# Kernel optimization log

Hardware: AMD Instinct MI355X
Metric: run time of the kernel (lower is better)

## Reference

```python
import jax, jax.numpy as jnp
import numpy as np

B, C_IN, C_OUT, H, W = 16, 256, 256, 64, 64
RANK, ORDER = 16, 2
EPS = 1e-5


def setup_inputs() -> dict:
    key = jax.random.key(0)
    k1, k2, k3 = jax.random.split(key, 3)
    x = jax.random.normal(k1, (B, C_IN, H, W), dtype=jnp.float32)
    # torch init: w_core ~ N(0, 1/(C_in*rank)), w_out ~ N(0, 1/rank)
    w_core = jax.random.normal(k2, (RANK, C_IN, RANK), dtype=jnp.float32) * (1.0 / (C_IN * RANK))
    w_out = jax.random.normal(k3, (RANK, C_OUT, RANK), dtype=jnp.float32) * (1.0 / RANK)
    return {"x": x, "w_core": w_core, "w_out": w_out}


def reference(x, w_core, w_out):
    # Per-pixel tensor-ring 1x1 conv.
    # Original chain for order=2 (share_core):
    #   T = einsum('achw,rck->arhwk', x, w_core)
    #   out = einsum('aebcf,afbcg,gdh->aedbch', T, T, w_out)
    #   y   = einsum('arohwr->aohw', out)   # ring trace over e==h
    # Equivalent: M[a,h,w] is rank x rank; P = M^order; y_d = tr(P @ W_d)
    M = jnp.einsum('achw,rck->ahwrk', x, w_core)  # [B,H,W,r,r]
    P = M
    for _ in range(ORDER - 1):
        P = jnp.einsum('ahwef,ahwfg->ahweg', P, M)
    y = jnp.einsum('ahweg,gde->adhw', P, w_out)  # [B,C_out,H,W]
    # InstanceNorm2d (affine=False, biased variance) + Softsign
    mean = jnp.mean(y, axis=(2, 3), keepdims=True)
    var = jnp.var(y, axis=(2, 3), keepdims=True)
    yn = (y - mean) * jax.lax.rsqrt(var + EPS)
    return yn / (1.0 + jnp.abs(yn))
```

## Files before the change

kernel.cpp:

```cpp
#include <hip/hip_runtime.h>

#define HW 4096
#define NC 256
#define ND 256
#define NB 16

typedef _Float16 half2_t __attribute__((ext_vector_type(2)));
typedef _Float16 half4_t __attribute__((ext_vector_type(4)));
typedef _Float16 half8_t __attribute__((ext_vector_type(8)));
typedef __fp16   fp16x2  __attribute__((ext_vector_type(2)));
typedef float floatx2 __attribute__((ext_vector_type(2)));
typedef float floatx4 __attribute__((ext_vector_type(4)));

#define MSCALE 64.0f
#define INV_MSCALE2 (1.0f / 4096.0f)
#define EPS_SCALED (1e-5f * 4096.0f * 4096.0f)

__global__ __launch_bounds__(256) void prep_weights(
        const float* __restrict__ w_core, const float* __restrict__ w_out,
        _Float16* __restrict__ W1p, _Float16* __restrict__ W2p,
        float* __restrict__ ssum) {
    int tid = blockIdx.x * 256 + threadIdx.x;
    if (tid < 8192) ssum[tid] = 0.f;
    int l   = tid & 63;
    int rt  = (tid >> 6) & 15;
    int ks  = (tid >> 10) & 7;
    int sel = tid >> 13;
    int row = l & 15, kg = l >> 4;
    half8_t v;
    if (sel == 0) {
        int r = rt, k = row;
#pragma unroll
        for (int j = 0; j < 8; ++j) {
            int c = ks * 32 + kg * 8 + j;
            v[j] = (_Float16)(w_core[r * 4096 + c * 16 + k] * MSCALE);
        }
        *(half8_t*)&W1p[(size_t)((ks * 16 + rt) * 64 + l) * 8] = v;
    } else {
        int d = rt * 16 + row;
#pragma unroll
        for (int j = 0; j < 8; ++j) {
            int eg = ks * 32 + kg * 8 + j, e = eg >> 4, g = eg & 15;
            v[j] = (_Float16)w_out[g * 4096 + d * 16 + e];
        }
        *(half8_t*)&W2p[(size_t)((ks * 16 + rt) * 64 + l) * 8] = v;
    }
}

template<bool F16Y>
__global__ __launch_bounds__(256, 2) void compute_y(
        const float* __restrict__ x, const _Float16* __restrict__ W1p,
        const _Float16* __restrict__ W2p, float* __restrict__ y,
        _Float16* __restrict__ y16, float* __restrict__ ssum,
        float* __restrict__ ssq) {
    __shared__ __align__(16) float S[16384];
    _Float16* XT  = (_Float16*)S;
    float*    Mf  = S;
    _Float16* PLb = (_Float16*)S;

    const int t = threadIdx.x;
    const int l = t & 63, w = t >> 6;
    const int a = blockIdx.x >> 6;
    const int pixbase = (blockIdx.x & 63) * 64;
    const int row16 = l & 15, kg = l >> 4;
    const float* xa = x + (size_t)a * NC * HW + pixbase;

    {
        const int px = t & 63;
        const int o0 = t >> 6;
#pragma unroll
        for (int q = 0; q < 8; ++q) {
            const int oct = q * 4 + o0;
            half8_t hv;
#pragma unroll
            for (int j = 0; j < 8; ++j)
                hv[j] = (_Float16)xa[(size_t)(oct * 8 + j) * HW + px];
            *(half8_t*)&XT[px * 256 + ((oct ^ (px & 15)) << 3)] = hv;
        }
    }
    __syncthreads();

    floatx4 acc[4][4];
#pragma unroll
    for (int i = 0; i < 4; ++i)
#pragma unroll
        for (int j = 0; j < 4; ++j) acc[i][j] = (floatx4){0.f, 0.f, 0.f, 0.f};
    {
        const half8_t* W1v = (const half8_t*)W1p;
        half8_t af[4], afn[4];
#pragma unroll
        for (int rq = 0; rq < 4; ++rq) af[rq] = W1v[(w * 4 + rq) * 64 + l];
        for (int ks = 0; ks < 8; ++ks) {
            if (ks < 7) {
#pragma unroll
                for (int rq = 0; rq < 4; ++rq)
                    afn[rq] = W1v[((ks + 1) * 16 + w * 4 + rq) * 64 + l];
            }
#pragma unroll
            for (int pt = 0; pt < 4; ++pt) {
                const int px = pt * 16 + row16;
                half8_t bf = *(const half8_t*)
                    &XT[px * 256 + (((ks * 4 + kg) ^ row16) << 3)];
#pragma unroll
                for (int rq = 0; rq < 4; ++rq)
                    acc[rq][pt] = __builtin_amdgcn_mfma_f32_16x16x32_f16(
                                      af[rq], bf, acc[rq][pt], 0, 0, 0);
            }
#pragma unroll
            for (int rq = 0; rq < 4; ++rq) af[rq] = afn[rq];
        }
    }

    const half8_t* W2v = (const half8_t*)W2p;
    half8_t caf[4], cafn[4];
#pragma unroll
    for (int dq = 0; dq < 4; ++dq) caf[dq] = W2v[(w * 4 + dq) * 64 + l];

    __syncthreads();

#pragma unroll
    for (int rq = 0; rq < 4; ++rq) {
        const int u = (w * 4 + rq) * 4 + kg;
#pragma unroll
        for (int pt = 0; pt < 4; ++pt) {
            const int px = pt * 16 + row16;
            *(floatx4*)&Mf[px * 256 + ((u ^ row16) << 2)] = acc[rq][pt];
        }
    }
    __syncthreads();

    {
        const int p = t >> 2, qe = t & 3, ps = p & 15;
        const float* Mp = &Mf[p * 256];
        float Af[4][16];
#pragma unroll
        for (int i = 0; i < 4; ++i) {
            const int e = i * 4 + qe;
#pragma unroll
            for (int f4 = 0; f4 < 4; ++f4) {
                floatx4 v = *(const floatx4*)&Mp[(((e * 4 + f4) ^ ps) << 2)];
#pragma unroll
                for (int j = 0; j < 4; ++j) Af[i][f4 * 4 + j] = v[j];
            }
        }
        floatx2 Pacc[4][8];
#pragma unroll
        for (int i = 0; i < 4; ++i)
#pragma unroll
            for (int g2 = 0; g2 < 8; ++g2) Pacc[i][g2] = (floatx2){0.f, 0.f};
#pragma unroll
        for (int f = 0; f < 16; ++f) {
            floatx2 Bg[8];
#pragma unroll
            for (int g4 = 0; g4 < 4; ++g4) {
                floatx4 v = *(const floatx4*)&Mp[(((f * 4 + g4) ^ ps) << 2)];
                Bg[g4 * 2]     = (floatx2){v[0], v[1]};
                Bg[g4 * 2 + 1] = (floatx2){v[2], v[3]};
            }
#pragma unroll
            for (int i = 0; i < 4; ++i) {
                floatx2 a2 = {Af[i][f], Af[i][f]};
#pragma unroll
                for (int g2 = 0; g2 < 8; ++g2)
                    Pacc[i][g2] = __builtin_elementwise_fma(a2, Bg[g2], Pacc[i][g2]);
            }
        }
#pragma unroll
        for (int i = 0; i < 4; ++i) {
            const int e = i * 4 + qe;
#pragma unroll
            for (int h2 = 0; h2 < 2; ++h2) {
                half8_t hv;
#pragma unroll
                for (int g2 = 0; g2 < 4; ++g2) {
                    fp16x2 pk = __builtin_amdgcn_cvt_pkrtz(
                        Pacc[i][h2 * 4 + g2][0], Pacc[i][h2 * 4 + g2][1]);
                    hv[g2 * 2]     = (_Float16)pk[0];
                    hv[g2 * 2 + 1] = (_Float16)pk[1];
                }
                *(half8_t*)&PLb[p * 512 + (((e * 2 + h2) ^ ps) << 3)] = hv;
            }
        }
    }
    __syncthreads();

    floatx4 cacc[4][4];
#pragma unroll
    for (int i = 0; i < 4; ++i)
#pragma unroll
        for (int j = 0; j < 4; ++j) cacc[i][j] = (floatx4){0.f, 0.f, 0.f, 0.f};
    for (int ks = 0; ks < 8; ++ks) {
        if (ks < 7) {
#pragma unroll
            for (int dq = 0; dq < 4; ++dq)
                cafn[dq] = W2v[((ks + 1) * 16 + w * 4 + dq) * 64 + l];
        }
#pragma unroll
        for (int pt = 0; pt < 4; ++pt) {
            const int px = pt * 16 + row16;
            half8_t bf = *(const half8_t*)
                &PLb[px * 512 + (((ks * 4 + kg) ^ row16) << 3)];
#pragma unroll
            for (int dq = 0; dq < 4; ++dq)
                cacc[dq][pt] = __builtin_amdgcn_mfma_f32_16x16x32_f16(
                                   caf[dq], bf, cacc[dq][pt], 0, 0, 0);
        }
#pragma unroll
        for (int dq = 0; dq < 4; ++dq) caf[dq] = cafn[dq];
    }

    float*     ya   = y   + (size_t)a * ND * HW + pixbase;
    _Float16*  ya16 = F16Y ? (y16 + (size_t)a * ND * HW + pixbase) : nullptr;
#pragma unroll
    for (int dq = 0; dq < 4; ++dq) {
        const int dbase = (w * 4 + dq) * 16 + kg * 4;
#pragma unroll
        for (int r2 = 0; r2 < 4; ++r2) {
            const int d = dbase + r2;
            float s = 0.f, q2 = 0.f;
#pragma unroll
            for (int pt = 0; pt < 4; ++pt) {
                float v;
                if (F16Y) {
                    _Float16 hv = (_Float16)cacc[dq][pt][r2];
                    ya16[(size_t)d * HW + pt * 16 + row16] = hv;
                    v = (float)hv;
                } else {
                    v = cacc[dq][pt][r2] * INV_MSCALE2;
                    ya[(size_t)d * HW + pt * 16 + row16] = v;
                }
                s += v; q2 += v * v;
            }
#pragma unroll
            for (int off = 1; off < 16; off <<= 1) {
                s  += __shfl_xor(s, off);
                q2 += __shfl_xor(q2, off);
            }
            if (row16 == 0) {
                atomicAdd(&ssum[a * 256 + d], s);
                atomicAdd(&ssq [a * 256 + d], q2);
            }
        }
    }
}

__global__ __launch_bounds__(256) void finalize_f16(
        const _Float16* __restrict__ y16, const float* __restrict__ ssum,
        const float* __restrict__ ssq, float* __restrict__ out) {
    const int ad = blockIdx.x;
    const float m  = ssum[ad] * (1.f / HW);
    const float sv = ssq[ad] * (1.f / HW) - m * m;
    const float s  = rsqrtf(sv + EPS_SCALED);
    const size_t base = (size_t)ad * HW + threadIdx.x * 16;
    half8_t h0 = *(const half8_t*)&y16[base];
    half8_t h1 = *(const half8_t*)&y16[base + 8];
    float o[16];
#pragma unroll
    for (int j = 0; j < 8; ++j) {
        float z0 = ((float)h0[j] - m) * s;
        float z1 = ((float)h1[j] - m) * s;
        o[j]     = z0 / (1.f + fabsf(z0));
        o[8 + j] = z1 / (1.f + fabsf(z1));
    }
#pragma unroll
    for (int q = 0; q < 4; ++q)
        *(float4*)&out[base + q * 4] =
            make_float4(o[q * 4], o[q * 4 + 1], o[q * 4 + 2], o[q * 4 + 3]);
}

__global__ __launch_bounds__(256) void finalize_f32(
        float* __restrict__ y, const float* __restrict__ ssum,
        const float* __restrict__ ssq) {
    const int i4 = blockIdx.x * 256 + threadIdx.x;
    const int ad = i4 >> 10;
    const float m  = ssum[ad] * (1.f / HW);
    const float sv = ssq[ad] * (1.f / HW) - m * m;
    const float s  = rsqrtf(sv + 1e-5f);
    float4 v = ((const float4*)y)[i4];
    float vv[4] = {v.x, v.y, v.z, v.w};
#pragma unroll
    for (int lq = 0; lq < 4; ++lq) {
        float z = (vv[lq] - m) * s;
        vv[lq] = z / (1.f + fabsf(z));
    }
    ((float4*)y)[i4] = make_float4(vv[0], vv[1], vv[2], vv[3]);
}

extern "C" void kernel_launch(void* const* d_in, const int* in_sizes, int n_in,
                              void* d_out, int out_size, void* d_ws, size_t ws_size,
                              hipStream_t stream) {
    const float* x      = (const float*)d_in[0];
    const float* w_core = (const float*)d_in[1];
    const float* w_out  = (const float*)d_in[2];
    float* y = (float*)d_out;

    char* wsb = (char*)d_ws;
    _Float16* W1p = (_Float16*)wsb;
    _Float16* W2p = (_Float16*)(wsb + 131072);
    float* ssum   = (float*)(wsb + 262144);
    float* ssq    = (float*)(wsb + 278528);
    _Float16* y16 = (_Float16*)(wsb + 294912);

    const size_t need_f16 = 294912 + (size_t)NB * ND * HW * sizeof(_Float16);
    const bool use_f16 = ws_size >= need_f16;

    prep_weights<<<64, 256, 0, stream>>>(w_core, w_out, W1p, W2p, ssum);
    if (use_f16) {
        compute_y<true><<<1024, 256, 0, stream>>>(x, W1p, W2p, y, y16, ssum, ssq);
        finalize_f16<<<4096, 256, 0, stream>>>(y16, ssum, ssq, y);
    } else {
        compute_y<false><<<1024, 256, 0, stream>>>(x, W1p, W2p, y, nullptr, ssum, ssq);
        finalize_f32<<<16384, 256, 0, stream>>>(y, ssum, ssq);
    }
}
```

Before: 82.50 us.

## Store intermediate M in fp16 LDS to halve shared memory and batch x loads

The shared buffer shrinks from 64KB of float to 32KB of half, so M is stored as fp16 and converted back to float for the per-pixel 16x16 matrix square. This lowers LDS use per block and may allow more resident blocks. The x staging now issues 32 global loads before converting, which gives more memory-level parallelism, and the W1 fragment prefetch is hoisted ahead of the x load. Keeping M in fp16 loses some precision, and the restructured loops raise register pressure.

```diff
diff --git a/kernel.cpp b/kernel.cpp
--- a/kernel.cpp
+++ b/kernel.cpp
@@ -53,10 +53,7 @@
         const _Float16* __restrict__ W2p, float* __restrict__ y,
         _Float16* __restrict__ y16, float* __restrict__ ssum,
         float* __restrict__ ssq) {
-    __shared__ __align__(16) float S[16384];
-    _Float16* XT  = (_Float16*)S;
-    float*    Mf  = S;
-    _Float16* PLb = (_Float16*)S;
+    __shared__ __align__(16) _Float16 S[16384];
 
     const int t = threadIdx.x;
     const int l = t & 63, w = t >> 6;
@@ -65,17 +62,32 @@
     const int row16 = l & 15, kg = l >> 4;
     const float* xa = x + (size_t)a * NC * HW + pixbase;
 
+    const half8_t* W1v = (const half8_t*)W1p;
+    half8_t af[4], afn[4];
+#pragma unroll
+    for (int rq = 0; rq < 4; ++rq) af[rq] = W1v[(w * 4 + rq) * 64 + l];
+
     {
         const int px = t & 63;
         const int o0 = t >> 6;
 #pragma unroll
-        for (int q = 0; q < 8; ++q) {
-            const int oct = q * 4 + o0;
-            half8_t hv;
-#pragma unroll
-            for (int j = 0; j < 8; ++j)
-                hv[j] = (_Float16)xa[(size_t)(oct * 8 + j) * HW + px];
-            *(half8_t*)&XT[px * 256 + ((oct ^ (px & 15)) << 3)] = hv;
+        for (int h = 0; h < 2; ++h) {
+            float xr[32];
+#pragma unroll
+            for (int q = 0; q < 4; ++q) {
+                const int oct = (h * 4 + q) * 4 + o0;
+#pragma unroll
+                for (int j = 0; j < 8; ++j)
+                    xr[q * 8 + j] = xa[(size_t)(oct * 8 + j) * HW + px];
+            }
+#pragma unroll
+            for (int q = 0; q < 4; ++q) {
+                const int oct = (h * 4 + q) * 4 + o0;
+                half8_t hv;
+#pragma unroll
+                for (int j = 0; j < 8; ++j) hv[j] = (_Float16)xr[q * 8 + j];
+                *(half8_t*)&S[px * 256 + ((oct ^ (px & 15)) << 3)] = hv;
+            }
         }
     }
     __syncthreads();
@@ -85,30 +97,24 @@
     for (int i = 0; i < 4; ++i)
 #pragma unroll
         for (int j = 0; j < 4; ++j) acc[i][j] = (floatx4){0.f, 0.f, 0.f, 0.f};
-    {
-        const half8_t* W1v = (const half8_t*)W1p;
-        half8_t af[4], afn[4];
-#pragma unroll
-        for (int rq = 0; rq < 4; ++rq) af[rq] = W1v[(w * 4 + rq) * 64 + l];
-        for (int ks = 0; ks < 8; ++ks) {
-            if (ks < 7) {
-#pragma unroll
-                for (int rq = 0; rq < 4; ++rq)
-                    afn[rq] = W1v[((ks + 1) * 16 + w * 4 + rq) * 64 + l];
-            }
-#pragma unroll
-            for (int pt = 0; pt < 4; ++pt) {
-                const int px = pt * 16 + row16;
-                half8_t bf = *(const half8_t*)
-                    &XT[px * 256 + (((ks * 4 + kg) ^ row16) << 3)];
-#pragma unroll
-                for (int rq = 0; rq < 4; ++rq)
-                    acc[rq][pt] = __builtin_amdgcn_mfma_f32_16x16x32_f16(
-                                      af[rq], bf, acc[rq][pt], 0, 0, 0);
-            }
-#pragma unroll
-            for (int rq = 0; rq < 4; ++rq) af[rq] = afn[rq];
-        }
+    for (int ks = 0; ks < 8; ++ks) {
+        if (ks < 7) {
+#pragma unroll
+            for (int rq = 0; rq < 4; ++rq)
+                afn[rq] = W1v[((ks + 1) * 16 + w * 4 + rq) * 64 + l];
+        }
+#pragma unroll
+        for (int pt = 0; pt < 4; ++pt) {
+            const int px = pt * 16 + row16;
+            half8_t bf = *(const half8_t*)
+                &S[px * 256 + (((ks * 4 + kg) ^ row16) << 3)];
+#pragma unroll
+            for (int rq = 0; rq < 4; ++rq)
+                acc[rq][pt] = __builtin_amdgcn_mfma_f32_16x16x32_f16(
+                                  af[rq], bf, acc[rq][pt], 0, 0, 0);
+        }
+#pragma unroll
+        for (int rq = 0; rq < 4; ++rq) af[rq] = afn[rq];
     }
 
     const half8_t* W2v = (const half8_t*)W2p;
@@ -124,45 +130,52 @@
 #pragma unroll
         for (int pt = 0; pt < 4; ++pt) {
             const int px = pt * 16 + row16;
-            *(floatx4*)&Mf[px * 256 + ((u ^ row16) << 2)] = acc[rq][pt];
+            half4_t hv;
+#pragma unroll
+            for (int r2 = 0; r2 < 4; ++r2) hv[r2] = (_Float16)acc[rq][pt][r2];
+            *(half4_t*)&S[px * 256 + ((u ^ row16) << 2)] = hv;
         }
     }
     __syncthreads();
 
     {
         const int p = t >> 2, qe = t & 3, ps = p & 15;
-        const float* Mp = &Mf[p * 256];
-        float Af[4][16];
-#pragma unroll
-        for (int i = 0; i < 4; ++i) {
-            const int e = i * 4 + qe;
-#pragma unroll
-            for (int f4 = 0; f4 < 4; ++f4) {
-                floatx4 v = *(const floatx4*)&Mp[(((e * 4 + f4) ^ ps) << 2)];
-#pragma unroll
-                for (int j = 0; j < 4; ++j) Af[i][f4 * 4 + j] = v[j];
-            }
-        }
+        const _Float16* Mp = &S[p * 256];
         floatx2 Pacc[4][8];
 #pragma unroll
         for (int i = 0; i < 4; ++i)
 #pragma unroll
             for (int g2 = 0; g2 < 8; ++g2) Pacc[i][g2] = (floatx2){0.f, 0.f};
 #pragma unroll
-        for (int f = 0; f < 16; ++f) {
-            floatx2 Bg[8];
-#pragma unroll
-            for (int g4 = 0; g4 < 4; ++g4) {
-                floatx4 v = *(const floatx4*)&Mp[(((f * 4 + g4) ^ ps) << 2)];
-                Bg[g4 * 2]     = (floatx2){v[0], v[1]};
-                Bg[g4 * 2 + 1] = (floatx2){v[2], v[3]};
-            }
+        for (int f4 = 0; f4 < 4; ++f4) {
+            float Afb[4][4];
 #pragma unroll
             for (int i = 0; i < 4; ++i) {
-                floatx2 a2 = {Af[i][f], Af[i][f]};
-#pragma unroll
-                for (int g2 = 0; g2 < 8; ++g2)
-                    Pacc[i][g2] = __builtin_elementwise_fma(a2, Bg[g2], Pacc[i][g2]);
+                const int e = i * 4 + qe;
+                half4_t v = *(const half4_t*)
+                    &Mp[(((e * 4 + f4) ^ ps) << 2)];
+#pragma unroll
+                for (int j = 0; j < 4; ++j) Afb[i][j] = (float)v[j];
+            }
+#pragma unroll
+            for (int fl = 0; fl < 4; ++fl) {
+                const int f = f4 * 4 + fl;
+                floatx2 Bg[8];
+#pragma unroll
+                for (int g4 = 0; g4 < 4; ++g4) {
+                    half4_t v = *(const half4_t*)
+                        &Mp[(((f * 4 + g4) ^ ps) << 2)];
+                    Bg[g4 * 2]     = (floatx2){(float)v[0], (float)v[1]};
+                    Bg[g4 * 2 + 1] = (floatx2){(float)v[2], (float)v[3]};
+                }
+#pragma unroll
+                for (int i = 0; i < 4; ++i) {
+                    floatx2 a2 = {Afb[i][fl], Afb[i][fl]};
+#pragma unroll
+                    for (int g2 = 0; g2 < 8; ++g2)
+                        Pacc[i][g2] = __builtin_elementwise_fma(a2, Bg[g2],
+                                                                Pacc[i][g2]);
+                }
             }
         }
 #pragma unroll
@@ -178,7 +191,7 @@
                     hv[g2 * 2]     = (_Float16)pk[0];
                     hv[g2 * 2 + 1] = (_Float16)pk[1];
                 }
-                *(half8_t*)&PLb[p * 512 + (((e * 2 + h2) ^ ps) << 3)] = hv;
+                *(half8_t*)&S[p * 256 + (((e * 2 + h2) ^ ps) << 3)] = hv;
             }
         }
     }
@@ -199,7 +212,7 @@
         for (int pt = 0; pt < 4; ++pt) {
             const int px = pt * 16 + row16;
             half8_t bf = *(const half8_t*)
-                &PLb[px * 512 + (((ks * 4 + kg) ^ row16) << 3)];
+                &S[px * 256 + (((ks * 4 + kg) ^ row16) << 3)];
 #pragma unroll
             for (int dq = 0; dq < 4; ++dq)
                 cacc[dq][pt] = __builtin_amdgcn_mfma_f32_16x16x32_f16(
```

After: 81.26 us. Within noise of the previous version (-1.5%).
